# Kernel optimization log

Measured on AMD Instinct MI355X. Metric: run time of the kernel, lower is better.

The kernel has to match this reference:

```python
import jax, jax.numpy as jnp
import numpy as np

N_NODES = 100000
N_EDGES = 3200000
D_IN = 128
HEADS = 8
F_OUT = 64


def setup_inputs() -> dict:
    key = jax.random.key(0)
    k1, k2, k3, k4, k5, k6 = jax.random.split(key, 6)
    node_features = jax.random.normal(k1, (N_NODES, D_IN), dtype=jnp.float32)
    linear_proj = jax.random.normal(k2, (D_IN, HEADS * F_OUT), dtype=jnp.float32) * (1.0 / np.sqrt(D_IN))
    scoring_fn_source = jax.random.normal(k3, (1, HEADS, F_OUT), dtype=jnp.float32) * 0.1
    scoring_fn_target = jax.random.normal(k4, (1, HEADS, F_OUT), dtype=jnp.float32) * 0.1
    edge_index = jax.random.randint(k5, (2, N_EDGES), 0, N_NODES, dtype=jnp.int64)
    return {
        'node_features': node_features,
        'linear_proj': linear_proj,
        'scoring_fn_source': scoring_fn_source,
        'scoring_fn_target': scoring_fn_target,
        'edge_index': edge_index,
    }


def reference(node_features, linear_proj, scoring_fn_source, scoring_fn_target, edge_index):
    # node_features: [N, D_in]; edge_index: [2, E] (row 0 = src, row 1 = trg)
    N = node_features.shape[0]
    H, F = scoring_fn_source.shape[1], scoring_fn_source.shape[2]

    # linear projection: [N, H, F]
    proj = (node_features @ linear_proj).reshape(N, H, F)

    # per-node attention scores: [N, H]
    scores_source = jnp.sum(proj * scoring_fn_source, axis=-1)
    scores_target = jnp.sum(proj * scoring_fn_target, axis=-1)

    src, trg = edge_index[0], edge_index[1]
    # lift to edges + LeakyReLU: [E, H]
    scores_per_edge = jax.nn.leaky_relu(scores_source[src] + scores_target[trg],
                                        negative_slope=0.2)

    # neighborhood-aware softmax over edges sharing the same target node
    seg_max = jax.ops.segment_max(scores_per_edge, trg, num_segments=N)   # [N, H]
    exp_scores = jnp.exp(scores_per_edge - seg_max[trg])                  # [E, H]
    seg_sum = jax.ops.segment_sum(exp_scores, trg, num_segments=N)        # [N, H]
    attentions_per_edge = exp_scores / (seg_sum[trg] + 1e-16)             # [E, H]
    return attentions_per_edge
```

## Files before the change

### kernel.cpp

```cpp
#include <hip/hip_runtime.h>
#include <hip/hip_fp16.h>

#define D_IN   128
#define HEADS  8
#define FOUT   64
#define NOUT   16
#define NPB    512
#define NPB_SH 9
#define NB_MAX 1024
#define CHUNK  8192
#define NBLK_MAX 1024
#define TPN    8
#define SROWS  64
#define SPAD   129
#define DET_BLOCKS 128

typedef unsigned __attribute__((ext_vector_type(2))) uint2v;
typedef float    __attribute__((ext_vector_type(4))) float4v;

__device__ __forceinline__ unsigned pack2(float a, float b) {
    union { __half2 h; unsigned u; } c;
    c.h = __floats2half2_rn(a, b);
    return c.u;
}
__device__ __forceinline__ float2 up2(unsigned u) {
    union { unsigned x; __half2 h; } c;
    c.x = u;
    return __half22float2(c.h);
}

__device__ __forceinline__ unsigned ntl_u(const unsigned* p) {
    return __builtin_nontemporal_load(p);
}
__device__ __forceinline__ uint2v ntl_u2(const unsigned* p) {
    return __builtin_nontemporal_load((const uint2v*)p);
}
__device__ __forceinline__ float4v ntl_f4(const float* p) {
    return __builtin_nontemporal_load((const float4v*)p);
}
__device__ __forceinline__ void nts_f4(float* p, float4v v) {
    __builtin_nontemporal_store(v, (float4v*)p);
}

__device__ __forceinline__ void load_edge(const unsigned int* idx, int e, int E,
                                          bool is64, unsigned int& s, unsigned int& t) {
    if (is64) {
        uint2v a = ntl_u2(idx + 2 * (size_t)e);
        uint2v b = ntl_u2(idx + 2 * ((size_t)E + e));
        s = a.x; t = b.x;
    } else {
        s = ntl_u(idx + e);
        t = ntl_u(idx + (size_t)E + e);
    }
}

__global__ void k_fold_w(const float* __restrict__ W,
                         const float* __restrict__ a_src,
                         const float* __restrict__ a_trg,
                         float* __restrict__ Wc,
                         unsigned int* __restrict__ flag,
                         int* __restrict__ binTotal, int NB) {
    int t = blockIdx.x * blockDim.x + threadIdx.x;
    if (t == 0) { flag[0] = 0u; flag[1] = 1u; }
    if (t < NB) binTotal[t] = 0;
    if (t >= D_IN * HEADS) return;
    int d = t >> 3, h = t & 7;
    const float* wrow = W + d * (HEADS * FOUT) + h * FOUT;
    float s1 = 0.f, s2 = 0.f;
    #pragma unroll 4
    for (int f = 0; f < FOUT; ++f) {
        float w = wrow[f];
        s1 += w * a_src[h * FOUT + f];
        s2 += w * a_trg[h * FOUT + f];
    }
    Wc[h * D_IN + d]           = s1;
    Wc[(HEADS + h) * D_IN + d] = s2;
}

__global__ void k_scores_t(const float* __restrict__ x,
                           const float* __restrict__ Wc,
                           float* __restrict__ ssrc_f,
                           float* __restrict__ strg_f,
                           __half* __restrict__ ssrc_h, int N,
                           const unsigned int* __restrict__ idx_w, int dwords,
                           unsigned int* __restrict__ flag) {
    if (blockIdx.x < DET_BLOCKS) {
        unsigned int local = 0;
        int stride = DET_BLOCKS * 256;
        for (int i = blockIdx.x * 256 + threadIdx.x; 2 * i + 1 < dwords; i += stride)
            local |= idx_w[2 * i + 1];
        if (__any(local != 0) && (threadIdx.x & 63) == 0)
            atomicOr(flag, 1u);
    }

    __shared__ float xt[SROWS * SPAD];
    int node0 = blockIdx.x * SROWS;
    int tid   = threadIdx.x;
    int nrows = min(SROWS, N - node0);

    for (int i = tid; i < nrows * 32; i += 256) {
        int r = i >> 5, c = (i & 31) * 4;
        float4v v = ntl_f4(x + (size_t)(node0 + r) * D_IN + c);
        float* dst = &xt[r * SPAD + c];
        dst[0] = v.x; dst[1] = v.y; dst[2] = v.z; dst[3] = v.w;
    }
    __syncthreads();

    int r  = tid & 63;
    int og = tid >> 6;
    if (r >= nrows) return;
    int n = node0 + r;

    const float* w = Wc + og * 4 * D_IN;
    float a0 = 0.f, a1 = 0.f, a2 = 0.f, a3 = 0.f;
    const float* xr = &xt[r * SPAD];
    #pragma unroll 8
    for (int d = 0; d < D_IN; ++d) {
        float xv = xr[d];
        a0 += xv * w[d];
        a1 += xv * w[D_IN + d];
        a2 += xv * w[2 * D_IN + d];
        a3 += xv * w[3 * D_IN + d];
    }

    if (og < 2) {
        if (ssrc_f)
            *(float4*)(ssrc_f + (size_t)n * HEADS + og * 4) =
                make_float4(a0, a1, a2, a3);
        uint2 hp;
        hp.x = pack2(a0, a1);
        hp.y = pack2(a2, a3);
        *(uint2*)(ssrc_h + (size_t)n * HEADS + og * 4) = hp;
    } else {
        *(float4*)(strg_f + (size_t)n * HEADS + (og - 2) * 4) =
            make_float4(a0, a1, a2, a3);
    }
}

__global__ void k_hist(const unsigned int* __restrict__ idx, int E,
                       const unsigned int* __restrict__ flag,
                       int* __restrict__ histB, int NB, int NBLK,
                       int* __restrict__ binTotal,
                       unsigned int* __restrict__ idx32) {
    __shared__ int h[NB_MAX];
    for (int i = threadIdx.x; i < NB; i += blockDim.x) h[i] = 0;
    __syncthreads();
    bool is64 = (*flag == 0u);
    int base = blockIdx.x * CHUNK;
    int lim  = min(base + CHUNK, E);
    for (int e = base + threadIdx.x; e < lim; e += blockDim.x) {
        unsigned int s, t;
        load_edge(idx, e, E, is64, s, t);
        if (idx32) {
            idx32[e]             = s;
            idx32[(size_t)E + e] = t;
        }
        atomicAdd(&h[t >> NPB_SH], 1);
    }
    __syncthreads();
    for (int i = threadIdx.x; i < NB; i += blockDim.x) {
        histB[(size_t)i * NBLK + blockIdx.x] = h[i];
        if (h[i]) atomicAdd(&binTotal[i], h[i]);
    }
}

__global__ void k_scan(const int* __restrict__ histB,
                       int* __restrict__ histA, int NB, int NBLK,
                       const int* __restrict__ binTotal,
                       int* __restrict__ binBase) {
    int b = blockIdx.x;
    int tid = threadIdx.x;
    if (b < NB) {
        __shared__ int v[NBLK_MAX];
        v[tid] = (tid < NBLK) ? histB[(size_t)b * NBLK + tid] : 0;
        __syncthreads();
        int w = 1; while (w < NBLK) w <<= 1;
        for (int off = 1; off < w; off <<= 1) {
            int t = (tid >= off) ? v[tid - off] : 0;
            __syncthreads();
            v[tid] += t;
            __syncthreads();
        }
        if (tid < NBLK)
            histA[(size_t)tid * NB + b] = tid ? v[tid - 1] : 0;
    } else {
        __shared__ int v2[NB_MAX];
        v2[tid] = (tid < NB) ? binTotal[tid] : 0;
        __syncthreads();
        int w = 1; while (w < NB) w <<= 1;
        for (int off = 1; off < w; off <<= 1) {
            int t = (tid >= off) ? v2[tid - off] : 0;
            __syncthreads();
            v2[tid] += t;
            __syncthreads();
        }
        if (tid < NB)
            binBase[tid] = tid ? v2[tid - 1] : 0;
    }
}

__global__ void k_scatter(const unsigned int* __restrict__ idx, int E,
                          const unsigned int* __restrict__ flag,
                          const int* __restrict__ histA, int NB,
                          const int* __restrict__ binBase,
                          unsigned int* __restrict__ binned) {
    __shared__ int cnt[NB_MAX];
    for (int i = threadIdx.x; i < NB; i += blockDim.x)
        cnt[i] = binBase[i] + histA[(size_t)blockIdx.x * NB + i];
    __syncthreads();
    bool is64 = (*flag == 0u);
    int base = blockIdx.x * CHUNK;
    int lim  = min(base + CHUNK, E);
    for (int e = base + threadIdx.x; e < lim; e += blockDim.x) {
        unsigned int s, t;
        load_edge(idx, e, E, is64, s, t);
        int pos = atomicAdd(&cnt[t >> NPB_SH], 1);
        binned[pos] = s | ((t & (NPB - 1u)) << 20);
    }
}

__global__ void k_sort2(const unsigned int* __restrict__ binned,
                        const int* __restrict__ binBase,
                        const int* __restrict__ binTotal,
                        unsigned int* __restrict__ sortedSrc,
                        int* __restrict__ rowPtr, int N, int NB) {
    __shared__ int cnt[NPB];
    __shared__ int scn[NPB];
    int b = blockIdx.x;
    int node0 = b << NPB_SH;
    int start = binBase[b], total = binTotal[b];
    int i = threadIdx.x;

    cnt[i] = 0;
    __syncthreads();
    for (int e = i; e < total; e += NPB)
        atomicAdd(&cnt[binned[start + e] >> 20], 1);
    __syncthreads();

    scn[i] = cnt[i];
    __syncthreads();
    for (int o = 1; o < NPB; o <<= 1) {
        int t = (i >= o) ? scn[i - o] : 0;
        __syncthreads();
        scn[i] += t;
        __syncthreads();
    }
    {
        int excl = scn[i] - cnt[i];
        cnt[i] = excl;
        int n = node0 + i;
        if (n < N) rowPtr[n] = start + excl;
    }
    if (b == NB - 1 && i == 0) rowPtr[N] = start + total;
    __syncthreads();

    for (int e = i; e < total; e += NPB) {
        unsigned int v = binned[start + e];
        int pos = atomicAdd(&cnt[v >> 20], 1);
        sortedSrc[start + pos] = v & 0xFFFFFu;
    }
}

__global__ void k_nodesum(const unsigned int* __restrict__ sortedSrc,
                          const int* __restrict__ rowPtr,
                          const __half* __restrict__ ssrc_h,
                          const float* __restrict__ strg_f,
                          __half* __restrict__ combo, int N) {
    int gt = blockIdx.x * blockDim.x + threadIdx.x;
    int n  = gt >> 3;
    int k  = gt & (TPN - 1);
    if (n >= N) return;

    int r0 = rowPtr[n], r1 = rowPtr[n + 1];
    const float4* tp = (const float4*)(strg_f + (size_t)n * HEADS);
    float4 ta = tp[0], tb = tp[1];
    float st[8] = { ta.x, ta.y, ta.z, ta.w, tb.x, tb.y, tb.z, tb.w };
    float acc[8] = { 0, 0, 0, 0, 0, 0, 0, 0 };

    for (int e = r0 + k; e < r1; e += TPN) {
        unsigned int s = sortedSrc[e];
        uint4 sv = *(const uint4*)(ssrc_h + (size_t)s * HEADS);
        float2 f01 = up2(sv.x), f23 = up2(sv.y), f45 = up2(sv.z), f67 = up2(sv.w);
        float vs[8] = { f01.x, f01.y, f23.x, f23.y, f45.x, f45.y, f67.x, f67.y };
        #pragma unroll
        for (int h = 0; h < HEADS; ++h) {
            float sc = vs[h] + st[h];
            sc = sc > 0.f ? sc : 0.2f * sc;
            acc[h] += expf(sc);
        }
    }
    #pragma unroll
    for (int h = 0; h < HEADS; ++h) {
        acc[h] += __shfl_xor(acc[h], 1, 64);
        acc[h] += __shfl_xor(acc[h], 2, 64);
        acc[h] += __shfl_xor(acc[h], 4, 64);
    }
    if (k == 0) {
        float rs[8];
        #pragma unroll
        for (int h = 0; h < HEADS; ++h) rs[h] = 1.0f / (acc[h] + 1e-16f);
        uint4 c0, c1;
        c0.x = pack2(st[0], st[1]);  c0.y = pack2(st[2], st[3]);
        c0.z = pack2(st[4], st[5]);  c0.w = pack2(st[6], st[7]);
        c1.x = pack2(rs[0], rs[1]);  c1.y = pack2(rs[2], rs[3]);
        c1.z = pack2(rs[4], rs[5]);  c1.w = pack2(rs[6], rs[7]);
        uint4* cp = (uint4*)(combo + (size_t)n * 16);
        cp[0] = c0;
        cp[1] = c1;
    }
}

__global__ void k_edge_out_c(const unsigned int* __restrict__ idx, int E,
                             const __half* __restrict__ ssrc_h,
                             const __half* __restrict__ combo,
                             const unsigned int* __restrict__ flag,
                             float* __restrict__ out) {
    int e = blockIdx.x * blockDim.x + threadIdx.x;
    if (e >= E) return;
    bool is64 = (*flag == 0u);
    unsigned int s, t;
    load_edge(idx, e, E, is64, s, t);

    uint4 sv = *(const uint4*)(ssrc_h + (size_t)s * HEADS);
    const uint4* cp = (const uint4*)(combo + (size_t)t * 16);
    uint4 c0 = cp[0], c1 = cp[1];

    float2 s01 = up2(sv.x), s23 = up2(sv.y), s45 = up2(sv.z), s67 = up2(sv.w);
    float2 t01 = up2(c0.x), t23 = up2(c0.y), t45 = up2(c0.z), t67 = up2(c0.w);
    float2 r01 = up2(c1.x), r23 = up2(c1.y), r45 = up2(c1.z), r67 = up2(c1.w);

    float ss[8] = { s01.x, s01.y, s23.x, s23.y, s45.x, s45.y, s67.x, s67.y };
    float st[8] = { t01.x, t01.y, t23.x, t23.y, t45.x, t45.y, t67.x, t67.y };
    float rs[8] = { r01.x, r01.y, r23.x, r23.y, r45.x, r45.y, r67.x, r67.y };

    float o[8];
    #pragma unroll
    for (int h = 0; h < HEADS; ++h) {
        float sc = ss[h] + st[h];
        sc = sc > 0.f ? sc : 0.2f * sc;
        o[h] = expf(sc) * rs[h];
    }
    float4v o0 = { o[0], o[1], o[2], o[3] };
    float4v o1 = { o[4], o[5], o[6], o[7] };
    nts_f4(out + (size_t)e * HEADS,     o0);
    nts_f4(out + (size_t)e * HEADS + 4, o1);
}

__device__ __forceinline__ void edge_scores(const float* ssrc, const float* strg,
                                            unsigned int s, unsigned int t, float* ex) {
    const float4* sp = (const float4*)(ssrc + (size_t)s * HEADS);
    const float4* tp = (const float4*)(strg + (size_t)t * HEADS);
    float4 sa = sp[0], sb = sp[1], ta = tp[0], tb = tp[1];
    float v[8] = { sa.x + ta.x, sa.y + ta.y, sa.z + ta.z, sa.w + ta.w,
                   sb.x + tb.x, sb.y + tb.y, sb.z + tb.z, sb.w + tb.w };
    #pragma unroll
    for (int h = 0; h < HEADS; ++h) {
        float sc = v[h];
        sc = sc > 0.f ? sc : 0.2f * sc;
        ex[h] = expf(sc);
    }
}

__global__ void k_detect_fb(const unsigned int* __restrict__ idx_w, int nwords,
                            unsigned int* __restrict__ flag) {
    unsigned int local = 0;
    int stride = gridDim.x * blockDim.x;
    for (int i = blockIdx.x * blockDim.x + threadIdx.x; 2 * i + 1 < nwords; i += stride)
        local |= idx_w[2 * i + 1];
    if (__any(local != 0) && (threadIdx.x & 63) == 0)
        atomicOr(flag, 1u);
}

__global__ void k_edge_sum(const unsigned int* __restrict__ idx, int E,
                           const float* __restrict__ ssrc,
                           const float* __restrict__ strg,
                           float* __restrict__ sums,
                           const unsigned int* __restrict__ flag) {
    int e = blockIdx.x * blockDim.x + threadIdx.x;
    if (e >= E) return;
    bool is64 = (*flag == 0u);
    unsigned int s, t;
    load_edge(idx, e, E, is64, s, t);
    float ex[8];
    edge_scores(ssrc, strg, s, t, ex);
    float* dst = sums + (size_t)t * HEADS;
    #pragma unroll
    for (int h = 0; h < HEADS; ++h)
        atomicAdd(dst + h, ex[h]);
}

__global__ void k_edge_out(const unsigned int* __restrict__ idx, int E,
                           const float* __restrict__ ssrc,
                           const float* __restrict__ strg,
                           const float* __restrict__ sums,
                           const unsigned int* __restrict__ flag,
                           float* __restrict__ out) {
    int e = blockIdx.x * blockDim.x + threadIdx.x;
    if (e >= E) return;
    bool is64 = (*flag == 0u);
    unsigned int s, t;
    load_edge(idx, e, E, is64, s, t);
    float ex[8];
    edge_scores(ssrc, strg, s, t, ex);
    const float4* sm = (const float4*)(sums + (size_t)t * HEADS);
    float4 m0 = sm[0], m1 = sm[1];
    float4 o0, o1;
    o0.x = ex[0] / (m0.x + 1e-16f);  o0.y = ex[1] / (m0.y + 1e-16f);
    o0.z = ex[2] / (m0.z + 1e-16f);  o0.w = ex[3] / (m0.w + 1e-16f);
    o1.x = ex[4] / (m1.x + 1e-16f);  o1.y = ex[5] / (m1.y + 1e-16f);
    o1.z = ex[6] / (m1.z + 1e-16f);  o1.w = ex[7] / (m1.w + 1e-16f);
    float4* op = (float4*)(out + (size_t)e * HEADS);
    op[0] = o0;
    op[1] = o1;
}

extern "C" void kernel_launch(void* const* d_in, const int* in_sizes, int n_in,
                              void* d_out, int out_size, void* d_ws, size_t ws_size,
                              hipStream_t stream) {
    const float*        x     = (const float*)d_in[0];
    const float*        W     = (const float*)d_in[1];
    const float*        a_src = (const float*)d_in[2];
    const float*        a_trg = (const float*)d_in[3];
    const unsigned int* idx   = (const unsigned int*)d_in[4];

    const int N  = in_sizes[0] / D_IN;
    const int E  = in_sizes[4] / 2;
    const int NH = N * HEADS;
    const int NB   = (N + NPB - 1) / NPB;
    const int NBLK = (E + CHUNK - 1) / CHUNK;

    float* out = (float*)d_out;
    char*  ws  = (char*)d_ws;
    size_t NHb = (size_t)NH * sizeof(float);

    size_t off = 0;
    auto alloc = [&](size_t bytes) { size_t o = off; off = (off + bytes + 255) & ~(size_t)255; return o; };
    unsigned int* flag     = (unsigned int*)(ws + alloc(8));
    float*        strg_f   = (float*)(ws + alloc(NHb));
    __half*       ssrc_h   = (__half*)(ws + alloc((size_t)NH * sizeof(__half)));
    __half*       combo    = (__half*)(ws + alloc((size_t)N * 16 * sizeof(__half)));
    float*        Wc       = (float*)(ws + alloc(NOUT * D_IN * sizeof(float)));
    int*          histA    = (int*)(ws + alloc((size_t)NBLK * NB * sizeof(int)));
    int*          histB    = (int*)(ws + alloc((size_t)NB * NBLK * sizeof(int)));
    int*          binTotal = (int*)(ws + alloc((size_t)NB * sizeof(int)));
    int*          binBase  = (int*)(ws + alloc((size_t)NB * sizeof(int)));
    unsigned int* binned   = (unsigned int*)(ws + alloc((size_t)E * sizeof(unsigned int)));
    unsigned int* sortedS  = (unsigned int*)(ws + alloc((size_t)E * sizeof(unsigned int)));
    int*          rowPtr   = (int*)(ws + alloc((size_t)(N + 1) * sizeof(int)));
    size_t base_off = off;
    unsigned int* idx32    = (unsigned int*)(ws + alloc((size_t)2 * E * sizeof(unsigned int)));
    size_t full_off = off;

    const bool fast    = (base_off <= ws_size) && (NB <= NB_MAX) && (NBLK <= NBLK_MAX)
                         && (N < (1 << 20));
    const bool compact = fast && (full_off <= ws_size);

    int dwords = in_sizes[4];
    if (dwords > (1 << 20)) dwords = 1 << 20;

    if (fast) {
        const unsigned int* c_idx  = compact ? idx32    : idx;
        const unsigned int* c_flag = compact ? flag + 1 : flag;

        k_fold_w <<<(D_IN * HEADS + 255) / 256, 256, 0, stream>>>(W, a_src, a_trg, Wc,
                                                                  flag, binTotal, NB);
        k_scores_t <<<(N + SROWS - 1) / SROWS, 256, 0, stream>>>(x, Wc,
                                                                 (float*)nullptr,
                                                                 strg_f, ssrc_h, N,
                                                                 idx, dwords, flag);
        k_hist    <<<NBLK, 512, 0, stream>>>(idx, E, flag, histB, NB, NBLK, binTotal,
                                             compact ? idx32 : (unsigned int*)nullptr);
        k_scan    <<<NB + 1, NBLK_MAX, 0, stream>>>(histB, histA, NB, NBLK,
                                                    binTotal, binBase);
        k_scatter <<<NBLK, 512, 0, stream>>>(c_idx, E, c_flag, histA, NB, binBase,
                                             binned);
        k_sort2   <<<NB, NPB, 0, stream>>>(binned, binBase, binTotal, sortedS,
                                           rowPtr, N, NB);
        k_nodesum <<<(N * TPN + 511) / 512, 512, 0, stream>>>(sortedS, rowPtr,
                                                              ssrc_h, strg_f,
                                                              combo, N);
        k_edge_out_c <<<(E + 255) / 256, 256, 0, stream>>>(c_idx, E, ssrc_h, combo,
                                                           c_flag, out);
    } else {
        size_t o2 = 0;
        auto alloc2 = [&](size_t bytes) { size_t o = o2; o2 = (o2 + bytes + 255) & ~(size_t)255; return o; };
        unsigned int* fb_flag = (unsigned int*)(ws + alloc2(8));
        float*        fb_Wc   = (float*)(ws + alloc2(NOUT * D_IN * sizeof(float)));
        float*        fb_sums = (float*)(ws + alloc2(NHb));
        float*        fb_ssrc = (float*)(ws + alloc2(NHb));
        float*        fb_strg = (float*)(ws + alloc2(NHb));
        __half*       fb_ssh  = (__half*)(ws + alloc2((size_t)NH * sizeof(__half)));

        hipMemsetAsync(fb_sums, 0, NHb, stream);
        k_fold_w <<<(D_IN * HEADS + 255) / 256, 256, 0, stream>>>(W, a_src, a_trg,
                                                                  fb_Wc, fb_flag,
                                                                  (int*)nullptr, 0);
        k_detect_fb <<<128, 256, 0, stream>>>(idx, dwords, fb_flag);
        k_scores_t <<<(N + SROWS - 1) / SROWS, 256, 0, stream>>>(x, fb_Wc, fb_ssrc,
                                                                 fb_strg, fb_ssh, N,
                                                                 idx, 0, fb_flag);
        int eblocks = (E + 255) / 256;
        k_edge_sum <<<eblocks, 256, 0, stream>>>(idx, E, fb_ssrc, fb_strg, fb_sums,
                                                 fb_flag);
        k_edge_out <<<eblocks, 256, 0, stream>>>(idx, E, fb_ssrc, fb_strg, fb_sums,
                                                 fb_flag, out);
    }
}
```

Baseline: 220.4 us.

## Fuse histogram into scores kernel and drop compact idx32 copy

Merges the target-bin histogram pass into the node-score kernel. Each histogram block detects the index width locally from the first 64 words instead of waiting on the global flag. Removes the idx32 compaction that wrote a 32-bit copy of the edge list, so later passes read the original indices directly. Also runs the per-bin sort with 1024 threads and has each edge-output thread handle two edges. Together this saves a launch and a full write of the edge indices. In exchange, later passes read 64-bit indices again, and index-width detection now depends on a small sample.

```diff
diff --git a/kernel.cpp b/kernel.cpp
--- a/kernel.cpp
+++ b/kernel.cpp
@@ -61,8 +61,8 @@
                          unsigned int* __restrict__ flag,
                          int* __restrict__ binTotal, int NB) {
     int t = blockIdx.x * blockDim.x + threadIdx.x;
-    if (t == 0) { flag[0] = 0u; flag[1] = 1u; }
-    if (t < NB) binTotal[t] = 0;
+    if (t == 0) flag[0] = 0u;
+    if (binTotal && t < NB) binTotal[t] = 0;
     if (t >= D_IN * HEADS) return;
     int d = t >> 3, h = t & 7;
     const float* wrow = W + d * (HEADS * FOUT) + h * FOUT;
@@ -77,26 +77,57 @@
     Wc[(HEADS + h) * D_IN + d] = s2;
 }
 
-__global__ void k_scores_t(const float* __restrict__ x,
+__global__ void k_scores_h(const float* __restrict__ x,
                            const float* __restrict__ Wc,
-                           float* __restrict__ ssrc_f,
                            float* __restrict__ strg_f,
                            __half* __restrict__ ssrc_h, int N,
-                           const unsigned int* __restrict__ idx_w, int dwords,
-                           unsigned int* __restrict__ flag) {
-    if (blockIdx.x < DET_BLOCKS) {
+                           const unsigned int* __restrict__ idx, int E,
+                           int dwords, unsigned int* __restrict__ flag,
+                           int* __restrict__ histB, int NB, int NBLK,
+                           int* __restrict__ binTotal) {
+    int tid = threadIdx.x;
+
+    if ((int)blockIdx.x < DET_BLOCKS) {
         unsigned int local = 0;
         int stride = DET_BLOCKS * 256;
-        for (int i = blockIdx.x * 256 + threadIdx.x; 2 * i + 1 < dwords; i += stride)
-            local |= idx_w[2 * i + 1];
-        if (__any(local != 0) && (threadIdx.x & 63) == 0)
+        for (int i = blockIdx.x * 256 + tid; 2 * i + 1 < dwords; i += stride)
+            local |= idx[2 * i + 1];
+        if (__any(local != 0) && (tid & 63) == 0)
             atomicOr(flag, 1u);
+    }
+
+    if ((int)blockIdx.x < NBLK) {
+        __shared__ int h[NB_MAX];
+        __shared__ int s_i32;
+        if (tid == 0) s_i32 = 0;
+        for (int i = tid; i < NB; i += blockDim.x) h[i] = 0;
+        __syncthreads();
+        if (tid < 64) {
+            unsigned int v = (2 * tid + 1 < 2 * E) ? idx[2 * tid + 1] : 0u;
+            if (__any(v != 0) && tid == 0) s_i32 = 1;
+        }
+        __syncthreads();
+        bool is64 = (s_i32 == 0);
+
+        int base = blockIdx.x * CHUNK;
+        int lim  = min(base + CHUNK, E);
+        for (int e = base + tid; e < lim; e += blockDim.x) {
+            unsigned int t = is64 ? ntl_u2(idx + 2 * ((size_t)E + e)).x
+                                  : ntl_u(idx + (size_t)E + e);
+            atomicAdd(&h[t >> NPB_SH], 1);
+        }
+        __syncthreads();
+        for (int i = tid; i < NB; i += blockDim.x) {
+            histB[(size_t)i * NBLK + blockIdx.x] = h[i];
+            if (h[i]) atomicAdd(&binTotal[i], h[i]);
+        }
+        __syncthreads();
     }
 
     __shared__ float xt[SROWS * SPAD];
     int node0 = blockIdx.x * SROWS;
-    int tid   = threadIdx.x;
     int nrows = min(SROWS, N - node0);
+    if (nrows <= 0) return;
 
     for (int i = tid; i < nrows * 32; i += 256) {
         int r = i >> 5, c = (i & 31) * 4;
@@ -124,9 +155,6 @@
     }
 
     if (og < 2) {
-        if (ssrc_f)
-            *(float4*)(ssrc_f + (size_t)n * HEADS + og * 4) =
-                make_float4(a0, a1, a2, a3);
         uint2 hp;
         hp.x = pack2(a0, a1);
         hp.y = pack2(a2, a3);
@@ -134,33 +162,6 @@
     } else {
         *(float4*)(strg_f + (size_t)n * HEADS + (og - 2) * 4) =
             make_float4(a0, a1, a2, a3);
-    }
-}
-
-__global__ void k_hist(const unsigned int* __restrict__ idx, int E,
-                       const unsigned int* __restrict__ flag,
-                       int* __restrict__ histB, int NB, int NBLK,
-                       int* __restrict__ binTotal,
-                       unsigned int* __restrict__ idx32) {
-    __shared__ int h[NB_MAX];
-    for (int i = threadIdx.x; i < NB; i += blockDim.x) h[i] = 0;
-    __syncthreads();
-    bool is64 = (*flag == 0u);
-    int base = blockIdx.x * CHUNK;
-    int lim  = min(base + CHUNK, E);
-    for (int e = base + threadIdx.x; e < lim; e += blockDim.x) {
-        unsigned int s, t;
-        load_edge(idx, e, E, is64, s, t);
-        if (idx32) {
-            idx32[e]             = s;
-            idx32[(size_t)E + e] = t;
-        }
-        atomicAdd(&h[t >> NPB_SH], 1);
-    }
-    __syncthreads();
-    for (int i = threadIdx.x; i < NB; i += blockDim.x) {
-        histB[(size_t)i * NBLK + blockIdx.x] = h[i];
-        if (h[i]) atomicAdd(&binTotal[i], h[i]);
     }
 }
 
@@ -230,22 +231,23 @@
     int node0 = b << NPB_SH;
     int start = binBase[b], total = binTotal[b];
     int i = threadIdx.x;
-
-    cnt[i] = 0;
-    __syncthreads();
-    for (int e = i; e < total; e += NPB)
+    int T = blockDim.x;
+
+    if (i < NPB) cnt[i] = 0;
+    __syncthreads();
+    for (int e = i; e < total; e += T)
         atomicAdd(&cnt[binned[start + e] >> 20], 1);
     __syncthreads();
 
-    scn[i] = cnt[i];
+    if (i < NPB) scn[i] = cnt[i];
     __syncthreads();
     for (int o = 1; o < NPB; o <<= 1) {
-        int t = (i >= o) ? scn[i - o] : 0;
-        __syncthreads();
-        scn[i] += t;
-        __syncthreads();
-    }
-    {
+        int t = (i < NPB && i >= o) ? scn[i - o] : 0;
+        __syncthreads();
+        if (i < NPB) scn[i] += t;
+        __syncthreads();
+    }
+    if (i < NPB) {
         int excl = scn[i] - cnt[i];
         cnt[i] = excl;
         int n = node0 + i;
@@ -254,7 +256,7 @@
     if (b == NB - 1 && i == 0) rowPtr[N] = start + total;
     __syncthreads();
 
-    for (int e = i; e < total; e += NPB) {
+    for (int e = i; e < total; e += T) {
         unsigned int v = binned[start + e];
         int pos = atomicAdd(&cnt[v >> 20], 1);
         sortedSrc[start + pos] = v & 0xFFFFFu;
@@ -310,40 +312,59 @@
     }
 }
 
+__device__ __forceinline__ void edge_out_one(unsigned int s, unsigned int t,
+                                             const __half* __restrict__ ssrc_h,
+                                             const __half* __restrict__ combo,
+                                             float* o) {
+    uint4 sv = *(const uint4*)(ssrc_h + (size_t)s * HEADS);
+    const uint4* cp = (const uint4*)(combo + (size_t)t * 16);
+    uint4 c0 = cp[0], c1 = cp[1];
+    float2 s01 = up2(sv.x), s23 = up2(sv.y), s45 = up2(sv.z), s67 = up2(sv.w);
+    float2 t01 = up2(c0.x), t23 = up2(c0.y), t45 = up2(c0.z), t67 = up2(c0.w);
+    float2 r01 = up2(c1.x), r23 = up2(c1.y), r45 = up2(c1.z), r67 = up2(c1.w);
+    float ss[8] = { s01.x, s01.y, s23.x, s23.y, s45.x, s45.y, s67.x, s67.y };
+    float st[8] = { t01.x, t01.y, t23.x, t23.y, t45.x, t45.y, t67.x, t67.y };
+    float rs[8] = { r01.x, r01.y, r23.x, r23.y, r45.x, r45.y, r67.x, r67.y };
+    #pragma unroll
+    for (int h = 0; h < HEADS; ++h) {
+        float sc = ss[h] + st[h];
+        sc = sc > 0.f ? sc : 0.2f * sc;
+        o[h] = expf(sc) * rs[h];
+    }
+}
+
 __global__ void k_edge_out_c(const unsigned int* __restrict__ idx, int E,
                              const __half* __restrict__ ssrc_h,
                              const __half* __restrict__ combo,
                              const unsigned int* __restrict__ flag,
                              float* __restrict__ out) {
-    int e = blockIdx.x * blockDim.x + threadIdx.x;
-    if (e >= E) return;
+    int base = blockIdx.x * 512;
+    int t    = threadIdx.x;
+    int e0 = base + t;
+    int e1 = base + t + 256;
+    if (e0 >= E) return;
     bool is64 = (*flag == 0u);
-    unsigned int s, t;
-    load_edge(idx, e, E, is64, s, t);
-
-    uint4 sv = *(const uint4*)(ssrc_h + (size_t)s * HEADS);
-    const uint4* cp = (const uint4*)(combo + (size_t)t * 16);
-    uint4 c0 = cp[0], c1 = cp[1];
-
-    float2 s01 = up2(sv.x), s23 = up2(sv.y), s45 = up2(sv.z), s67 = up2(sv.w);
-    float2 t01 = up2(c0.x), t23 = up2(c0.y), t45 = up2(c0.z), t67 = up2(c0.w);
-    float2 r01 = up2(c1.x), r23 = up2(c1.y), r45 = up2(c1.z), r67 = up2(c1.w);
-
-    float ss[8] = { s01.x, s01.y, s23.x, s23.y, s45.x, s45.y, s67.x, s67.y };
-    float st[8] = { t01.x, t01.y, t23.x, t23.y, t45.x, t45.y, t67.x, t67.y };
-    float rs[8] = { r01.x, r01.y, r23.x, r23.y, r45.x, r45.y, r67.x, r67.y };
-
-    float o[8];
-    #pragma unroll
-    for (int h = 0; h < HEADS; ++h) {
-        float sc = ss[h] + st[h];
-        sc = sc > 0.f ? sc : 0.2f * sc;
-        o[h] = expf(sc) * rs[h];
-    }
-    float4v o0 = { o[0], o[1], o[2], o[3] };
-    float4v o1 = { o[4], o[5], o[6], o[7] };
-    nts_f4(out + (size_t)e * HEADS,     o0);
-    nts_f4(out + (size_t)e * HEADS + 4, o1);
+    bool v1 = e1 < E;
+
+    unsigned int s0, t0, s1, t1;
+    load_edge(idx, e0, E, is64, s0, t0);
+    int e1c = v1 ? e1 : e0;
+    load_edge(idx, e1c, E, is64, s1, t1);
+
+    float o0[8], o1[8];
+    edge_out_one(s0, t0, ssrc_h, combo, o0);
+    edge_out_one(s1, t1, ssrc_h, combo, o1);
+
+    float4v a0 = { o0[0], o0[1], o0[2], o0[3] };
+    float4v a1 = { o0[4], o0[5], o0[6], o0[7] };
+    nts_f4(out + (size_t)e0 * HEADS,     a0);
+    nts_f4(out + (size_t)e0 * HEADS + 4, a1);
+    if (v1) {
+        float4v b0 = { o1[0], o1[1], o1[2], o1[3] };
+        float4v b1 = { o1[4], o1[5], o1[6], o1[7] };
+        nts_f4(out + (size_t)e1 * HEADS,     b0);
+        nts_f4(out + (size_t)e1 * HEADS + 4, b1);
+    }
 }
 
 __device__ __forceinline__ void edge_scores(const float* ssrc, const float* strg,
@@ -369,6 +390,44 @@
         local |= idx_w[2 * i + 1];
     if (__any(local != 0) && (threadIdx.x & 63) == 0)
         atomicOr(flag, 1u);
+}
+
+__global__ void k_scores_fb(const float* __restrict__ x,
+                            const float* __restrict__ Wc,
+                            float* __restrict__ ssrc_f,
+                            float* __restrict__ strg_f, int N) {
+    __shared__ float xt[SROWS * SPAD];
+    int node0 = blockIdx.x * SROWS;
+    int tid   = threadIdx.x;
+    int nrows = min(SROWS, N - node0);
+
+    for (int i = tid; i < nrows * 32; i += 256) {
+        int r = i >> 5, c = (i & 31) * 4;
+        float4v v = ntl_f4(x + (size_t)(node0 + r) * D_IN + c);
+        float* dst = &xt[r * SPAD + c];
+        dst[0] = v.x; dst[1] = v.y; dst[2] = v.z; dst[3] = v.w;
+    }
+    __syncthreads();
+
+    int r  = tid & 63;
+    int og = tid >> 6;
+    if (r >= nrows) return;
+    int n = node0 + r;
+
+    const float* w = Wc + og * 4 * D_IN;
+    float a0 = 0.f, a1 = 0.f, a2 = 0.f, a3 = 0.f;
+    const float* xr = &xt[r * SPAD];
+    #pragma unroll 8
+    for (int d = 0; d < D_IN; ++d) {
+        float xv = xr[d];
+        a0 += xv * w[d];
+        a1 += xv * w[D_IN + d];
+        a2 += xv * w[2 * D_IN + d];
+        a3 += xv * w[3 * D_IN + d];
+    }
+    float4 res = make_float4(a0, a1, a2, a3);
+    if (og < 2) *(float4*)(ssrc_f + (size_t)n * HEADS + og * 4)       = res;
+    else        *(float4*)(strg_f + (size_t)n * HEADS + (og - 2) * 4) = res;
 }
 
 __global__ void k_edge_sum(const unsigned int* __restrict__ idx, int E,
@@ -447,40 +506,32 @@
     unsigned int* binned   = (unsigned int*)(ws + alloc((size_t)E * sizeof(unsigned int)));
     unsigned int* sortedS  = (unsigned int*)(ws + alloc((size_t)E * sizeof(unsigned int)));
     int*          rowPtr   = (int*)(ws + alloc((size_t)(N + 1) * sizeof(int)));
-    size_t base_off = off;
-    unsigned int* idx32    = (unsigned int*)(ws + alloc((size_t)2 * E * sizeof(unsigned int)));
-    size_t full_off = off;
-
-    const bool fast    = (base_off <= ws_size) && (NB <= NB_MAX) && (NBLK <= NBLK_MAX)
-                         && (N < (1 << 20));
-    const bool compact = fast && (full_off <= ws_size);
+
+    const bool fast = (off <= ws_size) && (NB <= NB_MAX) && (NBLK <= NBLK_MAX)
+                      && (N < (1 << 20));
 
     int dwords = in_sizes[4];
     if (dwords > (1 << 20)) dwords = 1 << 20;
 
     if (fast) {
-        const unsigned int* c_idx  = compact ? idx32    : idx;
-        const unsigned int* c_flag = compact ? flag + 1 : flag;
-
         k_fold_w <<<(D_IN * HEADS + 255) / 256, 256, 0, stream>>>(W, a_src, a_trg, Wc,
                                                                   flag, binTotal, NB);
-        k_scores_t <<<(N + SROWS - 1) / SROWS, 256, 0, stream>>>(x, Wc,
-                                                                 (float*)nullptr,
-                                                                 strg_f, ssrc_h, N,
-                                                                 idx, dwords, flag);
-        k_hist    <<<NBLK, 512, 0, stream>>>(idx, E, flag, histB, NB, NBLK, binTotal,
-                                             compact ? idx32 : (unsigned int*)nullptr);
+        k_scores_h <<<(N + SROWS - 1) / SROWS, 256, 0, stream>>>(x, Wc, strg_f,
+                                                                 ssrc_h, N, idx, E,
+                                                                 dwords, flag,
+                                                                 histB, NB, NBLK,
+                                                                 binTotal);
         k_scan    <<<NB + 1, NBLK_MAX, 0, stream>>>(histB, histA, NB, NBLK,
                                                     binTotal, binBase);
-        k_scatter <<<NBLK, 512, 0, stream>>>(c_idx, E, c_flag, histA, NB, binBase,
+        k_scatter <<<NBLK, 512, 0, stream>>>(idx, E, flag, histA, NB, binBase,
                                              binned);
-        k_sort2   <<<NB, NPB, 0, stream>>>(binned, binBase, binTotal, sortedS,
-                                           rowPtr, N, NB);
+        k_sort2   <<<NB, 1024, 0, stream>>>(binned, binBase, binTotal, sortedS,
+                                            rowPtr, N, NB);
         k_nodesum <<<(N * TPN + 511) / 512, 512, 0, stream>>>(sortedS, rowPtr,
                                                               ssrc_h, strg_f,
                                                               combo, N);
-        k_edge_out_c <<<(E + 255) / 256, 256, 0, stream>>>(c_idx, E, ssrc_h, combo,
-                                                           c_flag, out);
+        k_edge_out_c <<<(E + 511) / 512, 256, 0, stream>>>(idx, E, ssrc_h, combo,
+                                                           flag, out);
     } else {
         size_t o2 = 0;
         auto alloc2 = [&](size_t bytes) { size_t o = o2; o2 = (o2 + bytes + 255) & ~(size_t)255; return o; };
@@ -489,16 +540,14 @@
         float*        fb_sums = (float*)(ws + alloc2(NHb));
         float*        fb_ssrc = (float*)(ws + alloc2(NHb));
         float*        fb_strg = (float*)(ws + alloc2(NHb));
-        __half*       fb_ssh  = (__half*)(ws + alloc2((size_t)NH * sizeof(__half)));
 
         hipMemsetAsync(fb_sums, 0, NHb, stream);
         k_fold_w <<<(D_IN * HEADS + 255) / 256, 256, 0, stream>>>(W, a_src, a_trg,
                                                                   fb_Wc, fb_flag,
                                                                   (int*)nullptr, 0);
         k_detect_fb <<<128, 256, 0, stream>>>(idx, dwords, fb_flag);
-        k_scores_t <<<(N + SROWS - 1) / SROWS, 256, 0, stream>>>(x, fb_Wc, fb_ssrc,
-                                                                 fb_strg, fb_ssh, N,
-                                                                 idx, 0, fb_flag);
+        k_scores_fb <<<(N + SROWS - 1) / SROWS, 256, 0, stream>>>(x, fb_Wc, fb_ssrc,
+                                                                  fb_strg, N);
         int eblocks = (E + 255) / 256;
         k_edge_sum <<<eblocks, 256, 0, stream>>>(idx, E, fb_ssrc, fb_strg, fb_sums,
                                                  fb_flag);
```

Result: faster. 214.4 us (-2.7%).
